# Kernel tuning notes

Measured on AMD Instinct MI355X. Metric: run time of the kernel, lower is better.

The kernel has to match this reference:

```python
import jax, jax.numpy as jnp
import numpy as np

B, T, C, HS = 4, 4096, 1024, 128

def setup_inputs() -> dict:
    key = jax.random.key(0)
    kx, kq, kk, kv = jax.random.split(key, 4)
    x = jax.random.normal(kx, (B, T, C), dtype=jnp.float32)
    # bias-free Linear weights, stored as (in, out) so projection is x @ W
    scale = 1.0 / np.sqrt(C)
    Wq = jax.random.normal(kq, (C, HS), dtype=jnp.float32) * scale
    Wk = jax.random.normal(kk, (C, HS), dtype=jnp.float32) * scale
    Wv = jax.random.normal(kv, (C, HS), dtype=jnp.float32) * scale
    return {"x": x, "Wq": Wq, "Wk": Wk, "Wv": Wv}

def reference(x, Wq, Wk, Wv):
    # x: (B,T,C) -> q,k,v: (B,T,HS)
    q = jnp.einsum('btc,ch->bth', x, Wq)
    k = jnp.einsum('btc,ch->bth', x, Wk)
    v = jnp.einsum('btc,ch->bth', x, Wv)
    hs = k.shape[-1]
    # scaled scores (B,T,T) with causal mask
    wei = jnp.einsum('bth,bsh->bts', q, k) * (hs ** -0.5)
    causal = jnp.tril(jnp.ones((q.shape[1], q.shape[1]), dtype=bool))
    wei = jnp.where(causal, wei, -jnp.inf)
    wei = jax.nn.softmax(wei, axis=-1)
    # dropout p=0.0 -> identity
    out = jnp.einsum('bts,bsh->bth', wei, v)
    return out
```

## Files before the change

### kernel.cpp

```cpp
#include <hip/hip_runtime.h>
#include <hip/hip_bf16.h>

typedef __attribute__((ext_vector_type(8))) short short8;
typedef __attribute__((ext_vector_type(4))) short s4v;
typedef __attribute__((ext_vector_type(4))) float f32x4;

#define BATCH 4
#define TLEN 4096
#define CDIM 1024
#define HSD 128
#define MROWS (BATCH*TLEN)

#define QSCALE 0.12751744f

#ifdef __HIP_DEVICE_COMPILE__
  #define MFMA16(a,b,c) __builtin_amdgcn_mfma_f32_16x16x16bf16_1k(a,b,c,0,0,0)
#else
  #define MFMA16(a,b,c) (c)
#endif

__device__ __forceinline__ unsigned short f2bf(float f){
    unsigned u = __builtin_bit_cast(unsigned, f);
    u = (u + 0x7FFFu + ((u >> 16) & 1u)) >> 16;
    return (unsigned short)u;
}
__device__ __forceinline__ unsigned pkbf(float a, float b){
    unsigned ua = (__builtin_bit_cast(unsigned, a) + 0x8000u) >> 16;
    unsigned ub = (__builtin_bit_cast(unsigned, b) + 0x8000u) & 0xFFFF0000u;
    return ua | ub;
}

__global__ void prep_w_k(const float* __restrict__ Wq, const float* __restrict__ Wk,
                         const float* __restrict__ Wv, unsigned short* __restrict__ Wt){
    int idx = blockIdx.x * 256 + threadIdx.x;
    const int total = 3 * HSD * CDIM;
    if (idx >= total) return;
    int w = idx / (HSD * CDIM);
    int r = idx - w * HSD * CDIM;
    int h = r / CDIM;
    int c = r - h * CDIM;
    const float* W = (w == 0) ? Wq : ((w == 1) ? Wk : Wv);
    Wt[idx] = f2bf(W[c * HSD + h]);
}

__device__ __forceinline__ void stage_w_tile(unsigned short* buf, const unsigned short* g,
                                             int tid){
#pragma unroll
    for (int i = 0; i < 2; i++){
        int c = i * 256 + tid;
        int row = c >> 2, kp = c & 3;
        int swz = (row & 3) ^ ((row >> 2) & 3);
        const unsigned short* gp = g + (size_t)row * CDIM + ((kp ^ swz) << 3);
        unsigned short* lp = buf + (c << 3);
        __builtin_amdgcn_global_load_lds((const __attribute__((address_space(1))) void*)gp,
                                         (__attribute__((address_space(3))) void*)lp, 16, 0, 0);
    }
}

__global__ __launch_bounds__(256) void proj_k(const float* __restrict__ x,
                                              const unsigned short* __restrict__ Wt,
                                              unsigned short* __restrict__ Qb,
                                              unsigned short* __restrict__ Kb,
                                              unsigned short* __restrict__ Vt){
    __shared__ unsigned short As[2][64 * 32];
    __shared__ unsigned short Bs[2][128 * 32];

    const int tid = threadIdx.x, lane = tid & 63, wave = tid >> 6;
    const int m = lane & 15, quad = lane >> 4;
    const int wr = wave & 1, wc = wave >> 1;
    const int rb = blockIdx.x * 64;
    const int p  = blockIdx.y;

    const float* gA = x + (size_t)rb * CDIM;
    const unsigned short* gB = Wt + (size_t)(p * HSD) * CDIM;

    const int arow = tid >> 2, ach = tid & 3;
    const int aswz = (arow & 3) ^ ((arow >> 2) & 3);
    const int agc = ach ^ aswz;
    const float* agp = gA + (size_t)arow * CDIM + (agc << 3);

    f32x4 acc[4][4];
#pragma unroll
    for (int i = 0; i < 4; i++)
#pragma unroll
        for (int j = 0; j < 4; j++) acc[i][j] = (f32x4)0.f;

    stage_w_tile(&Bs[0][0], gB, tid);
    {
        float4 a0 = *(const float4*)(agp);
        float4 a1 = *(const float4*)(agp + 4);
        short8 o;
        o[0]=(short)f2bf(a0.x); o[1]=(short)f2bf(a0.y); o[2]=(short)f2bf(a0.z); o[3]=(short)f2bf(a0.w);
        o[4]=(short)f2bf(a1.x); o[5]=(short)f2bf(a1.y); o[6]=(short)f2bf(a1.z); o[7]=(short)f2bf(a1.w);
        *(short8*)&As[0][arow * 32 + (ach << 3)] = o;
    }
    __syncthreads();

    int cur = 0;
    for (int kc = 0; kc < CDIM / 32; ++kc){
        float4 a0n, a1n;
        if (kc + 1 < CDIM / 32){
            stage_w_tile(&Bs[cur ^ 1][0], gB + (kc + 1) * 32, tid);
            a0n = *(const float4*)(agp + (kc + 1) * 32);
            a1n = *(const float4*)(agp + (kc + 1) * 32 + 4);
        }
        if (p < 2){
            short8 aF[4], bF[2];
#pragma unroll
            for (int i = 0; i < 4; i++){
                int ra = wr * 64 + i * 16 + m;
                int sa = (ra & 3) ^ ((ra >> 2) & 3);
                aF[i] = *(const short8*)&Bs[cur][ra * 32 + ((quad ^ sa) << 3)];
            }
#pragma unroll
            for (int j = 0; j < 2; j++){
                int rn = wc * 32 + j * 16 + m;
                int sb = (rn & 3) ^ ((rn >> 2) & 3);
                bF[j] = *(const short8*)&As[cur][rn * 32 + ((quad ^ sb) << 3)];
            }
#pragma unroll
            for (int i = 0; i < 4; i++)
#pragma unroll
                for (int j = 0; j < 2; j++)
                    acc[i][j] = __builtin_amdgcn_mfma_f32_16x16x32_bf16(aF[i], bF[j], acc[i][j], 0, 0, 0);
        } else {
            short8 aF[2], bF[4];
#pragma unroll
            for (int i = 0; i < 2; i++){
                int ra = wr * 32 + i * 16 + m;
                int sa = (ra & 3) ^ ((ra >> 2) & 3);
                aF[i] = *(const short8*)&As[cur][ra * 32 + ((quad ^ sa) << 3)];
            }
#pragma unroll
            for (int j = 0; j < 4; j++){
                int rn = wc * 64 + j * 16 + m;
                int sb = (rn & 3) ^ ((rn >> 2) & 3);
                bF[j] = *(const short8*)&Bs[cur][rn * 32 + ((quad ^ sb) << 3)];
            }
#pragma unroll
            for (int i = 0; i < 2; i++)
#pragma unroll
                for (int j = 0; j < 4; j++)
                    acc[i][j] = __builtin_amdgcn_mfma_f32_16x16x32_bf16(aF[i], bF[j], acc[i][j], 0, 0, 0);
        }
        if (kc + 1 < CDIM / 32){
            short8 o;
            o[0]=(short)f2bf(a0n.x); o[1]=(short)f2bf(a0n.y); o[2]=(short)f2bf(a0n.z); o[3]=(short)f2bf(a0n.w);
            o[4]=(short)f2bf(a1n.x); o[5]=(short)f2bf(a1n.y); o[6]=(short)f2bf(a1n.z); o[7]=(short)f2bf(a1n.w);
            *(short8*)&As[cur ^ 1][arow * 32 + (ach << 3)] = o;
        }
        __syncthreads();
        cur ^= 1;
    }

    if (p < 2){
        unsigned short* D = (p == 0) ? Qb : Kb;
        const float qs = (p == 0) ? QSCALE : 1.0f;
#pragma unroll
        for (int i = 0; i < 4; i++){
#pragma unroll
            for (int j = 0; j < 2; j++){
                int h = wr * 64 + i * 16 + quad * 4;
                int t = rb + wc * 32 + j * 16 + m;
                ushort4 v;
                v.x = f2bf(acc[i][j][0] * qs); v.y = f2bf(acc[i][j][1] * qs);
                v.z = f2bf(acc[i][j][2] * qs); v.w = f2bf(acc[i][j][3] * qs);
                *(ushort4*)(D + (size_t)t * HSD + h) = v;
            }
        }
    } else {
        int b = rb >> 12;
        int tb = rb & 4095;
#pragma unroll
        for (int i = 0; i < 2; i++){
#pragma unroll
            for (int j = 0; j < 4; j++){
                int t = tb + wr * 32 + i * 16 + quad * 4;
                int h = wc * 64 + j * 16 + m;
                ushort4 v;
                v.x = f2bf(acc[i][j][0]); v.y = f2bf(acc[i][j][1]);
                v.z = f2bf(acc[i][j][2]); v.w = f2bf(acc[i][j][3]);
                *(ushort4*)(Vt + ((size_t)b * HSD + h) * TLEN + t) = v;
            }
        }
    }
}

__global__ __launch_bounds__(256, 3) void attn_k(const unsigned short* __restrict__ Qb,
                       const unsigned short* __restrict__ Kb,
                       const unsigned short* __restrict__ Vts,
                       float* __restrict__ Opart, float* __restrict__ lpart, int seglen){
    __shared__ unsigned short Kf[16 * 512];
    __shared__ unsigned short Vf[32 * 256];

    const int tid = threadIdx.x, lane = tid & 63, wave = tid >> 6;
    const int m = lane & 15, quad = lane >> 4;
    const int q0 = ((int)gridDim.x - 1 - (int)blockIdx.x) * 128;
    const int seg = blockIdx.y, b = blockIdx.z;
    const int g0 = seg * seglen;
    if (g0 >= q0 + 128) return;
    const int gend = min(g0 + seglen, q0 + 128);
    const int nT = (gend - g0) >> 6;

    const int q0w = q0 + wave * 32;
    const size_t rowg = (size_t)b * TLEN + q0w;

    short8 aQ[2][4];
#pragma unroll
    for (int h = 0; h < 2; h++)
#pragma unroll
        for (int kk = 0; kk < 4; kk++)
            aQ[h][kk] = *(const short8*)(Qb + (rowg + h * 16 + m) * HSD + kk * 32 + quad * 8);

    f32x4 accO[2][8];
#pragma unroll
    for (int h = 0; h < 2; h++)
#pragma unroll
        for (int i = 0; i < 8; i++) accO[h][i] = (f32x4)0.f;
    float lp0 = 0.f, lp1 = 0.f;

    const unsigned short* kbase = Kb + (size_t)b * TLEN * HSD;
    const unsigned short* vbase = Vts + (size_t)b * HSD * TLEN;

    int koff[4];
#pragma unroll
    for (int i = 0; i < 4; i++){
        int s = i * 256 + tid;
        int g = s >> 6, l = s & 63;
        int ns = g >> 2, kk = g & 3, qd = l >> 4, mm = l & 15;
        koff[i] = (16 * ns + mm) * HSD + kk * 32 + qd * 8;
    }
    int voff[4], vdst[4];
#pragma unroll
    for (int i = 0; i < 4; i++){
        int c = i * 256 + tid;
        int mm = c & 15, sc = (c >> 4) & 7, hi = c >> 7;
        voff[i] = (hi * 16 + mm) * TLEN + sc * 8;
        int ns = sc >> 1, qa = (sc & 1) * 2;
        vdst[i] = ((hi * 4 + ns) * 64 + qa * 16 + mm) * 4;
    }

    const unsigned short* kl = Kf + lane * 8;
    const unsigned short* vl = Vf + lane * 4;

    for (int t = 0; t < nT; ++t){
        const int s0 = g0 + t * 64;
        const unsigned short* kt = kbase + (size_t)s0 * HSD;
#pragma unroll
        for (int i = 0; i < 4; i++){
            __builtin_amdgcn_global_load_lds(
                (const __attribute__((address_space(1))) void*)(kt + koff[i]),
                (__attribute__((address_space(3))) void*)(Kf + (size_t)(i * 256 + tid) * 8),
                16, 0, 0);
        }
        uint4 vv[4];
#pragma unroll
        for (int i = 0; i < 4; i++)
            vv[i] = *(const uint4*)(vbase + voff[i] + s0);
#pragma unroll
        for (int i = 0; i < 4; i++){
            *(uint2*)&Vf[vdst[i]]      = make_uint2(vv[i].x, vv[i].y);
            *(uint2*)&Vf[vdst[i] + 64] = make_uint2(vv[i].z, vv[i].w);
        }
        __syncthreads();

        if (s0 <= q0w + 31){
            s4v aP[2][4];
#pragma unroll
            for (int ns = 0; ns < 4; ns++){
                short8 kf[4];
#pragma unroll
                for (int kk = 0; kk < 4; kk++)
                    kf[kk] = *(const short8*)(kl + (ns * 4 + kk) * 512);
#pragma unroll
                for (int h = 0; h < 2; h++){
                    f32x4 sa = (f32x4)0.f;
#pragma unroll
                    for (int kk = 0; kk < 4; kk++)
                        sa = __builtin_amdgcn_mfma_f32_16x16x32_bf16(kf[kk], aQ[h][kk], sa, 0, 0, 0);
                    if (s0 + 63 > q0w){
                        int qg = q0w + h * 16 + m;
#pragma unroll
                        for (int r = 0; r < 4; r++){
                            int sg = s0 + ns * 16 + quad * 4 + r;
                            if (sg > qg) sa[r] = -1e30f;
                        }
                    }
                    float p0 = exp2f(sa[0]), p1 = exp2f(sa[1]);
                    float p2 = exp2f(sa[2]), p3 = exp2f(sa[3]);
                    if (h == 0) lp0 += (p0 + p1) + (p2 + p3);
                    else        lp1 += (p0 + p1) + (p2 + p3);
                    uint2 u;
                    u.x = pkbf(p0, p1);
                    u.y = pkbf(p2, p3);
                    aP[h][ns] = __builtin_bit_cast(s4v, u);
                }
            }
#pragma unroll
            for (int sub = 0; sub < 8; sub++){
#pragma unroll
                for (int ns = 0; ns < 4; ns++){
                    s4v bV = *(const s4v*)(vl + (sub * 4 + ns) * 256);
                    accO[0][sub] = MFMA16(aP[0][ns], bV, accO[0][sub]);
                    accO[1][sub] = MFMA16(aP[1][ns], bV, accO[1][sub]);
                }
            }
        }
        __syncthreads();
    }
    lp0 += __shfl_xor(lp0, 16, 64);
    lp0 += __shfl_xor(lp0, 32, 64);
    lp1 += __shfl_xor(lp1, 16, 64);
    lp1 += __shfl_xor(lp1, 32, 64);
    if (quad == 0){
        lpart[(size_t)seg * MROWS + rowg + m]      = lp0;
        lpart[(size_t)seg * MROWS + rowg + 16 + m] = lp1;
    }
    float* ob = Opart + (size_t)seg * MROWS * HSD;
#pragma unroll
    for (int h = 0; h < 2; h++)
#pragma unroll
        for (int sub = 0; sub < 8; sub++)
#pragma unroll
            for (int r = 0; r < 4; r++)
                ob[(rowg + h * 16 + quad * 4 + r) * HSD + sub * 16 + m] = accO[h][sub][r];
}

__global__ void merge_k(const float* __restrict__ Opart, const float* __restrict__ lpart,
                        float* __restrict__ out, int nseg, int seglen){
    int idx = blockIdx.x * 256 + threadIdx.x;
    int row = idx >> 7;
    int t = row & (TLEN - 1);
    int q0 = t & ~127;
    int nsv = min(nseg, (q0 + 127) / seglen + 1);
    float L = 0.f, o = 0.f;
    for (int s = 0; s < nsv; s++){
        L += lpart[(size_t)s * MROWS + row];
        o += Opart[(size_t)s * MROWS * HSD + idx];
    }
    out[idx] = o / L;
}

extern "C" void kernel_launch(void* const* d_in, const int* in_sizes, int n_in,
                              void* d_out, int out_size, void* d_ws, size_t ws_size,
                              hipStream_t stream) {
    const float* x  = (const float*)d_in[0];
    const float* Wq = (const float*)d_in[1];
    const float* Wk = (const float*)d_in[2];
    const float* Wv = (const float*)d_in[3];
    float* out = (float*)d_out;
    char* w = (char*)d_ws;

    unsigned short* Wt = (unsigned short*)w;
    unsigned short* Qb = (unsigned short*)(w + ((size_t)1u  << 20));
    unsigned short* Kb = (unsigned short*)(w + ((size_t)5u  << 20));
    unsigned short* Vt = (unsigned short*)(w + ((size_t)9u  << 20));
    float* lpart       = (float*)(w + ((size_t)13u << 20));
    float* Opart;
    int nseg;
    const size_t segbytes = (size_t)MROWS * HSD * 4;
    if (ws_size >= ((size_t)14u << 20) + 8 * segbytes){
        nseg = 8;  Opart = (float*)(w + ((size_t)14u << 20));
    } else if (ws_size >= ((size_t)14u << 20) + 4 * segbytes){
        nseg = 4;  Opart = (float*)(w + ((size_t)14u << 20));
    } else {
        nseg = 1;  Opart = out;
    }
    const int seglen = TLEN / nseg;

    prep_w_k<<<(3 * HSD * CDIM + 255) / 256, 256, 0, stream>>>(Wq, Wk, Wv, Wt);
    proj_k<<<dim3(MROWS / 64, 3), 256, 0, stream>>>(x, Wt, Qb, Kb, Vt);
    attn_k<<<dim3(TLEN / 128, nseg, BATCH), 256, 0, stream>>>(Qb, Kb, Vt, Opart, lpart, seglen);
    merge_k<<<(MROWS * HSD) / 256, 256, 0, stream>>>(Opart, lpart, out, nseg, seglen);
}
```

Before: 209.9 us.

## Finer split-K attention segments with bf16 partials and MFMA row sums

Attention now splits the key dimension into finer chunks: up to 16 segments of 256 keys, chosen from the workspace size. This gives more and better-balanced blocks over the causal triangle, and blocks are no longer launched in reversed order. Partial outputs are stored as bf16 instead of fp32 to halve the partial write and merge-read traffic. Softmax row sums are computed with an extra MFMA against a ones vector, which removes the scalar adds and shuffles. The launch-bounds occupancy hint is dropped. The cost is lower precision in the partial accumulators and extra MFMA work per tile.

Measured after the change: 265.1 us. 26.3% more time.

```diff
diff --git a/kernel.cpp b/kernel.cpp
--- a/kernel.cpp
+++ b/kernel.cpp
@@ -186,23 +186,24 @@
     }
 }
 
-__global__ __launch_bounds__(256, 3) void attn_k(const unsigned short* __restrict__ Qb,
+__global__ __launch_bounds__(256) void attn_k(const unsigned short* __restrict__ Qb,
                        const unsigned short* __restrict__ Kb,
                        const unsigned short* __restrict__ Vts,
-                       float* __restrict__ Opart, float* __restrict__ lpart, int seglen){
+                       unsigned short* __restrict__ Opart, float* __restrict__ lpart,
+                       int chk, int segmax){
     __shared__ unsigned short Kf[16 * 512];
     __shared__ unsigned short Vf[32 * 256];
 
     const int tid = threadIdx.x, lane = tid & 63, wave = tid >> 6;
     const int m = lane & 15, quad = lane >> 4;
-    const int q0 = ((int)gridDim.x - 1 - (int)blockIdx.x) * 128;
-    const int seg = blockIdx.y, b = blockIdx.z;
-    const int g0 = seg * seglen;
-    if (g0 >= q0 + 128) return;
-    const int gend = min(g0 + seglen, q0 + 128);
+    const int qt = blockIdx.x, s = blockIdx.y, b = blockIdx.z;
+    const int g0 = s * chk * 64;
+    const int qend = qt * 128 + 128;
+    if (g0 >= qend) return;
+    const int gend = min(g0 + chk * 64, qend);
     const int nT = (gend - g0) >> 6;
 
-    const int q0w = q0 + wave * 32;
+    const int q0w = qt * 128 + wave * 32;
     const size_t rowg = (size_t)b * TLEN + q0w;
 
     short8 aQ[2][4];
@@ -212,12 +213,14 @@
         for (int kk = 0; kk < 4; kk++)
             aQ[h][kk] = *(const short8*)(Qb + (rowg + h * 16 + m) * HSD + kk * 32 + quad * 8);
 
-    f32x4 accO[2][8];
-#pragma unroll
-    for (int h = 0; h < 2; h++)
+    f32x4 accO[2][8], accL[2];
+#pragma unroll
+    for (int h = 0; h < 2; h++){
+        accL[h] = (f32x4)0.f;
 #pragma unroll
         for (int i = 0; i < 8; i++) accO[h][i] = (f32x4)0.f;
-    float lp0 = 0.f, lp1 = 0.f;
+    }
+    const s4v vone = { (short)0x3F80, (short)0x3F80, (short)0x3F80, (short)0x3F80 };
 
     const unsigned short* kbase = Kb + (size_t)b * TLEN * HSD;
     const unsigned short* vbase = Vts + (size_t)b * HSD * TLEN;
@@ -225,8 +228,8 @@
     int koff[4];
 #pragma unroll
     for (int i = 0; i < 4; i++){
-        int s = i * 256 + tid;
-        int g = s >> 6, l = s & 63;
+        int sl = i * 256 + tid;
+        int g = sl >> 6, l = sl & 63;
         int ns = g >> 2, kk = g & 3, qd = l >> 4, mm = l & 15;
         koff[i] = (16 * ns + mm) * HSD + kk * 32 + qd * 8;
     }
@@ -239,7 +242,6 @@
         int ns = sc >> 1, qa = (sc & 1) * 2;
         vdst[i] = ((hi * 4 + ns) * 64 + qa * 16 + mm) * 4;
     }
-
     const unsigned short* kl = Kf + lane * 8;
     const unsigned short* vl = Vf + lane * 4;
 
@@ -288,8 +290,6 @@
                     }
                     float p0 = exp2f(sa[0]), p1 = exp2f(sa[1]);
                     float p2 = exp2f(sa[2]), p3 = exp2f(sa[3]);
-                    if (h == 0) lp0 += (p0 + p1) + (p2 + p3);
-                    else        lp1 += (p0 + p1) + (p2 + p3);
                     uint2 u;
                     u.x = pkbf(p0, p1);
                     u.y = pkbf(p2, p3);
@@ -297,6 +297,11 @@
                 }
             }
 #pragma unroll
+            for (int ns = 0; ns < 4; ns++){
+                accL[0] = MFMA16(aP[0][ns], vone, accL[0]);
+                accL[1] = MFMA16(aP[1][ns], vone, accL[1]);
+            }
+#pragma unroll
             for (int sub = 0; sub < 8; sub++){
 #pragma unroll
                 for (int ns = 0; ns < 4; ns++){
@@ -308,35 +313,40 @@
         }
         __syncthreads();
     }
-    lp0 += __shfl_xor(lp0, 16, 64);
-    lp0 += __shfl_xor(lp0, 32, 64);
-    lp1 += __shfl_xor(lp1, 16, 64);
-    lp1 += __shfl_xor(lp1, 32, 64);
-    if (quad == 0){
-        lpart[(size_t)seg * MROWS + rowg + m]      = lp0;
-        lpart[(size_t)seg * MROWS + rowg + 16 + m] = lp1;
-    }
-    float* ob = Opart + (size_t)seg * MROWS * HSD;
+    const size_t pbase = ((size_t)b * segmax + s) * TLEN + q0w;
+    if (m == 0){
+#pragma unroll
+        for (int h = 0; h < 2; h++)
+#pragma unroll
+            for (int r = 0; r < 4; r++)
+                lpart[pbase + h * 16 + quad * 4 + r] = accL[h][r];
+    }
+    unsigned short* ob = Opart + pbase * HSD;
 #pragma unroll
     for (int h = 0; h < 2; h++)
 #pragma unroll
         for (int sub = 0; sub < 8; sub++)
 #pragma unroll
             for (int r = 0; r < 4; r++)
-                ob[(rowg + h * 16 + quad * 4 + r) * HSD + sub * 16 + m] = accO[h][sub][r];
-}
-
-__global__ void merge_k(const float* __restrict__ Opart, const float* __restrict__ lpart,
-                        float* __restrict__ out, int nseg, int seglen){
+                ob[(h * 16 + quad * 4 + r) * HSD + sub * 16 + m] = f2bf(accO[h][sub][r]);
+}
+
+__global__ void merge_k(const unsigned short* __restrict__ Opart,
+                        const float* __restrict__ lpart,
+                        float* __restrict__ out, int chk, int segmax){
     int idx = blockIdx.x * 256 + threadIdx.x;
+    int h = idx & 127;
     int row = idx >> 7;
-    int t = row & (TLEN - 1);
-    int q0 = t & ~127;
-    int nsv = min(nseg, (q0 + 127) / seglen + 1);
+    int b = row >> 12;
+    int t = row & 4095;
+    int qt = t >> 7;
+    int nsv = (2 * qt + 2 + chk - 1) / chk;
     float L = 0.f, o = 0.f;
     for (int s = 0; s < nsv; s++){
-        L += lpart[(size_t)s * MROWS + row];
-        o += Opart[(size_t)s * MROWS * HSD + idx];
+        size_t base = ((size_t)b * segmax + s) * TLEN + t;
+        L += lpart[base];
+        unsigned u = Opart[base * HSD + h];
+        o += __builtin_bit_cast(float, u << 16);
     }
     out[idx] = o / L;
 }
@@ -356,20 +366,17 @@
     unsigned short* Kb = (unsigned short*)(w + ((size_t)5u  << 20));
     unsigned short* Vt = (unsigned short*)(w + ((size_t)9u  << 20));
     float* lpart       = (float*)(w + ((size_t)13u << 20));
-    float* Opart;
-    int nseg;
-    const size_t segbytes = (size_t)MROWS * HSD * 4;
-    if (ws_size >= ((size_t)14u << 20) + 8 * segbytes){
-        nseg = 8;  Opart = (float*)(w + ((size_t)14u << 20));
-    } else if (ws_size >= ((size_t)14u << 20) + 4 * segbytes){
-        nseg = 4;  Opart = (float*)(w + ((size_t)14u << 20));
-    } else {
-        nseg = 1;  Opart = out;
-    }
-    const int seglen = TLEN / nseg;
+    unsigned short* Opart = (unsigned short*)(w + ((size_t)14u << 20));
+
+    int chk, segmax;
+    const size_t segbytes = (size_t)MROWS * HSD * 2;
+    if      (ws_size >= ((size_t)14u << 20) + 16 * segbytes){ chk = 4;  segmax = 16; }
+    else if (ws_size >= ((size_t)14u << 20) +  8 * segbytes){ chk = 8;  segmax = 8;  }
+    else if (ws_size >= ((size_t)14u << 20) +  4 * segbytes){ chk = 16; segmax = 4;  }
+    else                                                    { chk = 64; segmax = 1;  }
 
     prep_w_k<<<(3 * HSD * CDIM + 255) / 256, 256, 0, stream>>>(Wq, Wk, Wv, Wt);
     proj_k<<<dim3(MROWS / 64, 3), 256, 0, stream>>>(x, Wt, Qb, Kb, Vt);
-    attn_k<<<dim3(TLEN / 128, nseg, BATCH), 256, 0, stream>>>(Qb, Kb, Vt, Opart, lpart, seglen);
-    merge_k<<<(MROWS * HSD) / 256, 256, 0, stream>>>(Opart, lpart, out, nseg, seglen);
-}
+    attn_k<<<dim3(32, segmax, BATCH), 256, 0, stream>>>(Qb, Kb, Vt, Opart, lpart, chk, segmax);
+    merge_k<<<(MROWS * HSD) / 256, 256, 0, stream>>>(Opart, lpart, out, chk, segmax);
+}
```
